# Optimization experiments

Hardware: AMD Instinct MI355X
Metric: run time of the kernel (lower is better)

Reference implementation:

```python
import jax, jax.numpy as jnp
import numpy as np

TOKENS = 64
IN_F = 8192
OUT_F = 8192
CODESZ = 8
CB_SIZE = 256


def fwht(x):
    """Sylvester fast Walsh-Hadamard transform along last dim. x: (B, n), n power of 2."""
    b, n = x.shape
    h = 1
    while h < n:
        x = x.reshape(b, n // (2 * h), 2, h)
        x = jnp.concatenate([x[:, :, :1] + x[:, :, 1:], x[:, :, :1] - x[:, :, 1:]], axis=2)
        x = x.reshape(b, n)
        h *= 2
    return x


def setup_inputs() -> dict:
    key = jax.random.key(0)
    k0, k1, k2, k3, k4, k5 = jax.random.split(key, 6)
    x = jax.random.normal(k0, (TOKENS, IN_F), jnp.float32)
    # SU/SV are random sign vectors in QuIP
    SU = jnp.sign(jax.random.normal(k1, (IN_F,), jnp.float32))
    SV = jnp.sign(jax.random.normal(k2, (OUT_F,), jnp.float32))
    grid = jax.random.normal(k3, (CB_SIZE, CODESZ), jnp.float32)  # codebook entries
    Wscale = jnp.ones((1,), jnp.float32)
    bias = jax.random.normal(k4, (OUT_F,), jnp.float32) * 0.01
    Qidxs = jax.random.randint(k5, (OUT_F, IN_F // CODESZ), 0, CB_SIZE, jnp.int32)
    return {"x": x, "SU": SU, "SV": SV, "grid": grid, "Wscale": Wscale, "bias": bias, "Qidxs": Qidxs}


def reference(x, SU, SV, grid, Wscale, bias, Qidxs):
    # 1) input sign scale
    xs = x * SU
    # 2) matmul_hadUt with folded wscale: x @ H^T / sqrt(n_in) * wscale (H symmetric Sylvester)
    inv_sqrt_in = 1.0 / jnp.sqrt(jnp.asarray(IN_F, x.dtype))
    xh = fwht(xs) * (inv_sqrt_in * Wscale[0])
    # 3) codebook dequant + matmul: W_hat[o, i] from codebook lookup, out = xh @ W_hat^T
    W_hat = grid[Qidxs].reshape(OUT_F, IN_F)  # (out, in) dequantized weight
    y = xh @ W_hat.T  # (tokens, out)
    # 4) matmul_hadU on the output side, truncate to out_features (no-op here: q_out == out)
    inv_sqrt_out = 1.0 / jnp.sqrt(jnp.asarray(OUT_F, x.dtype))
    yh = fwht(y) * inv_sqrt_out
    yh = yh[..., :OUT_F]
    # 5) output sign scale + bias
    return yh * SV + bias
```

## Files before the change

### kernel.cpp

```cpp
#include <hip/hip_runtime.h>
#include <hip/hip_bf16.h>

#define TOKENS 64
#define IN_F 8192
#define OUT_F 8192
#define CB 256

typedef _Float16 half8 __attribute__((ext_vector_type(8)));
typedef float f32x4 __attribute__((ext_vector_type(4)));

__global__ __launch_bounds__(256) void k_fwht_in(const float* __restrict__ x,
                                                 const float* __restrict__ SU,
                                                 const float* __restrict__ Wscale,
                                                 _Float16* __restrict__ xh_frag)
{
    __shared__ float buf[256 * 33];
    __shared__ _Float16 xrowP[256 * 40];
    const int t    = threadIdx.x;
    const int lane = t & 63;
    const int w    = t >> 6;
    const int row  = blockIdx.x;

    float v[32];
    const float* xr = x + row * IN_F;
#pragma unroll
    for (int r = 0; r < 32; ++r) {
        int e = r * 256 + t;
        v[r] = xr[e] * SU[e];
    }
#pragma unroll
    for (int h = 1; h < 32; h <<= 1) {
#pragma unroll
        for (int r = 0; r < 32; ++r) {
            if ((r & h) == 0) {
                float a = v[r], b = v[r + h];
                v[r] = a + b;
                v[r + h] = a - b;
            }
        }
    }
#pragma unroll
    for (int m = 1; m < 64; m <<= 1) {
        bool upper = (lane & m) != 0;
#pragma unroll
        for (int r = 0; r < 32; ++r) {
            float p = __shfl_xor(v[r], m, 64);
            v[r] = upper ? (p - v[r]) : (v[r] + p);
        }
    }
#pragma unroll
    for (int r = 0; r < 32; ++r) buf[t * 33 + r] = v[r];
    __syncthreads();
    {
        float s1 = (w & 1) ? -1.f : 1.f;
        float s2 = (w & 2) ? -1.f : 1.f;
        float s3 = s1 * s2;
#pragma unroll
        for (int r = 0; r < 32; ++r) {
            float a0 = buf[(0 * 64 + lane) * 33 + r];
            float a1 = buf[(1 * 64 + lane) * 33 + r];
            float a2 = buf[(2 * 64 + lane) * 33 + r];
            float a3 = buf[(3 * 64 + lane) * 33 + r];
            v[r] = a0 + s1 * a1 + s2 * a2 + s3 * a3;
        }
    }
    const float scale = 0.011048543456039806f * Wscale[0];
#pragma unroll
    for (int r = 0; r < 32; ++r) {
        int idx = (t & 31) + (r * 8 + (t >> 5)) * 40;
        xrowP[idx] = (_Float16)(v[r] * scale);
    }
    __syncthreads();
    {
        const int mt  = row >> 4;
        const int l15 = row & 15;
        _Float16* base = xh_frag + ((size_t)(t * 4 + mt) * 64 + l15) * 8;
#pragma unroll
        for (int g = 0; g < 4; ++g) {
            half8 val = *(const half8*)&xrowP[t * 40 + g * 8];
            *(half8*)(base + g * 16 * 8) = val;
        }
    }
}

#define SQ_STRIDE 261
__global__ __launch_bounds__(256, 2) void k_qgemm(const _Float16* __restrict__ xh_frag,
                                                  const int* __restrict__ Qidxs,
                                                  const float* __restrict__ grid,
                                                  float* __restrict__ y_part)
{
    __shared__ __align__(16) _Float16 glds[CB * 8];
    __shared__ __align__(16) char uni[4 * 64 * 68 * 4];
    int*   sq  = (int*)uni;
    float* red = (float*)uni;

    const int tid = threadIdx.x;
    const int g   = blockIdx.x >> 2;
    const int p   = blockIdx.x & 3;
    const int n0  = g * 64;

    {
        const float4* gp = (const float4*)grid + tid * 2;
        float4 g0 = gp[0];
        float4 g1 = gp[1];
        _Float16* gl = &glds[tid * 8];
        gl[0] = (_Float16)g0.x; gl[1] = (_Float16)g0.y;
        gl[2] = (_Float16)g0.z; gl[3] = (_Float16)g0.w;
        gl[4] = (_Float16)g1.x; gl[5] = (_Float16)g1.y;
        gl[6] = (_Float16)g1.z; gl[7] = (_Float16)g1.w;
    }
#pragma unroll
    for (int i = 0; i < 16; ++i) {
        int idx4 = i * 256 + tid;
        int r  = idx4 >> 6;
        int c4 = idx4 & 63;
        int4 vv = *(const int4*)(Qidxs + (size_t)(n0 + r) * 1024 + p * 256 + c4 * 4);
        int* dst = &sq[r * SQ_STRIDE + c4 * 4];
        dst[0] = vv.x; dst[1] = vv.y; dst[2] = vv.z; dst[3] = vv.w;
    }
    __syncthreads();

    const int lane = tid & 63;
    const int w    = tid >> 6;
    const int col  = lane & 15;
    const int quad = lane >> 4;

    const int cbase = w * 64 + quad;
#define QGATHER(dst4, s)                                              \
    {                                                                 \
        int cc = cbase + (s) * 4;                                     \
        dst4.x = sq[(0 * 16 + col) * SQ_STRIDE + cc];                 \
        dst4.y = sq[(1 * 16 + col) * SQ_STRIDE + cc];                 \
        dst4.z = sq[(2 * 16 + col) * SQ_STRIDE + cc];                 \
        dst4.w = sq[(3 * 16 + col) * SQ_STRIDE + cc];                 \
    }

    const _Float16* abase = xh_frag + ((size_t)(p * 64 + w * 16) * 4 * 64 + lane) * 8;

    f32x4 acc[4][4] = {};

    int4 qv1, qv2;
    half8 b_c[4];
    {
        int4 qv0;
        QGATHER(qv0, 0);
        QGATHER(qv1, 1);
        QGATHER(qv2, 2);
        b_c[0] = *(const half8*)&glds[qv0.x * 8];
        b_c[1] = *(const half8*)&glds[qv0.y * 8];
        b_c[2] = *(const half8*)&glds[qv0.z * 8];
        b_c[3] = *(const half8*)&glds[qv0.w * 8];
    }
    half8 a_c[4], a_n[4];
#pragma unroll
    for (int mt = 0; mt < 4; ++mt) {
        a_c[mt] = *(const half8*)(abase + (size_t)(0 * 4 + mt) * 512);
        a_n[mt] = *(const half8*)(abase + (size_t)(1 * 4 + mt) * 512);
    }

#pragma unroll 4
    for (int s = 0; s < 16; ++s) {
        const int s3 = (s + 3 < 16 ? s + 3 : 15);
        const int s2 = (s + 2 < 16 ? s + 2 : 15);
        int4 qn;
        QGATHER(qn, s3);
        half8 b_n[4], a_nn[4];
        b_n[0] = *(const half8*)&glds[qv1.x * 8];
        b_n[1] = *(const half8*)&glds[qv1.y * 8];
        b_n[2] = *(const half8*)&glds[qv1.z * 8];
        b_n[3] = *(const half8*)&glds[qv1.w * 8];
#pragma unroll
        for (int mt = 0; mt < 4; ++mt)
            a_nn[mt] = *(const half8*)(abase + (size_t)(s2 * 4 + mt) * 512);
#pragma unroll
        for (int nt = 0; nt < 4; ++nt)
#pragma unroll
            for (int mt = 0; mt < 4; ++mt)
                acc[nt][mt] = __builtin_amdgcn_mfma_f32_16x16x32_f16(
                    a_c[mt], b_c[nt], acc[nt][mt], 0, 0, 0);
#pragma unroll
        for (int nt = 0; nt < 4; ++nt) b_c[nt] = b_n[nt];
        qv1 = qv2; qv2 = qn;
#pragma unroll
        for (int mt = 0; mt < 4; ++mt) { a_c[mt] = a_n[mt]; a_n[mt] = a_nn[mt]; }
    }

    __syncthreads();
#pragma unroll
    for (int nt = 0; nt < 4; ++nt)
#pragma unroll
        for (int mt = 0; mt < 4; ++mt)
#pragma unroll
            for (int i = 0; i < 4; ++i) {
                int r = mt * 16 + quad * 4 + i;
                int c = nt * 16 + col;
                red[(w * 64 + r) * 68 + c] = acc[nt][mt][i];
            }
    __syncthreads();
    float* yp = y_part + (size_t)p * TOKENS * OUT_F;
#pragma unroll
    for (int j = 0; j < 16; ++j) {
        int idx = j * 256 + tid;
        int rr = idx >> 6, cc = idx & 63;
        float s = (red[(0 * 64 + rr) * 68 + cc] + red[(1 * 64 + rr) * 68 + cc])
                + (red[(2 * 64 + rr) * 68 + cc] + red[(3 * 64 + rr) * 68 + cc]);
        yp[(size_t)rr * OUT_F + n0 + cc] = s;
    }
#undef QGATHER
}

__global__ __launch_bounds__(256) void k_fwht_out(const float* __restrict__ y_part,
                                                  const float* __restrict__ SV,
                                                  const float* __restrict__ bias,
                                                  float* __restrict__ out)
{
    __shared__ float buf[256 * 33];
    const int t    = threadIdx.x;
    const int lane = t & 63;
    const int w    = t >> 6;
    const int row  = blockIdx.x;

    const float* y0 = y_part + (size_t)row * OUT_F;
    const size_t ps = (size_t)TOKENS * OUT_F;

    float v[32];
#pragma unroll
    for (int r = 0; r < 32; ++r) {
        int e = r * 256 + t;
        v[r] = (y0[e] + y0[e + ps]) + (y0[e + 2 * ps] + y0[e + 3 * ps]);
    }
#pragma unroll
    for (int h = 1; h < 32; h <<= 1) {
#pragma unroll
        for (int r = 0; r < 32; ++r) {
            if ((r & h) == 0) {
                float a = v[r], b = v[r + h];
                v[r] = a + b;
                v[r + h] = a - b;
            }
        }
    }
#pragma unroll
    for (int m = 1; m < 64; m <<= 1) {
        bool upper = (lane & m) != 0;
#pragma unroll
        for (int r = 0; r < 32; ++r) {
            float p = __shfl_xor(v[r], m, 64);
            v[r] = upper ? (p - v[r]) : (v[r] + p);
        }
    }
#pragma unroll
    for (int r = 0; r < 32; ++r) buf[t * 33 + r] = v[r];
    __syncthreads();
    {
        float s1 = (w & 1) ? -1.f : 1.f;
        float s2 = (w & 2) ? -1.f : 1.f;
        float s3 = s1 * s2;
#pragma unroll
        for (int r = 0; r < 32; ++r) {
            float a0 = buf[(0 * 64 + lane) * 33 + r];
            float a1 = buf[(1 * 64 + lane) * 33 + r];
            float a2 = buf[(2 * 64 + lane) * 33 + r];
            float a3 = buf[(3 * 64 + lane) * 33 + r];
            v[r] = a0 + s1 * a1 + s2 * a2 + s3 * a3;
        }
    }
    const float scale = 0.011048543456039806f;
    float* oo = out + (size_t)row * OUT_F;
#pragma unroll
    for (int r = 0; r < 32; ++r) {
        int e = r * 256 + t;
        oo[e] = v[r] * scale * SV[e] + bias[e];
    }
}

extern "C" void kernel_launch(void* const* d_in, const int* in_sizes, int n_in,
                              void* d_out, int out_size, void* d_ws, size_t ws_size,
                              hipStream_t stream) {
    const float* x      = (const float*)d_in[0];
    const float* SU     = (const float*)d_in[1];
    const float* SV     = (const float*)d_in[2];
    const float* grid   = (const float*)d_in[3];
    const float* Wscale = (const float*)d_in[4];
    const float* bias   = (const float*)d_in[5];
    const int*   Qidxs  = (const int*)d_in[6];
    float* out = (float*)d_out;

    _Float16* xh_frag = (_Float16*)d_ws;
    float*    y_part  = (float*)((char*)d_ws + ((size_t)1 << 20));

    k_fwht_in<<<TOKENS, 256, 0, stream>>>(x, SU, Wscale, xh_frag);
    k_qgemm<<<512, 256, 0, stream>>>(xh_frag, Qidxs, grid, y_part);
    k_fwht_out<<<TOKENS, 256, 0, stream>>>(y_part, SV, bias, out);
}
```

Baseline: 114.2 us.

## Stream Qidxs into per-wave LDS ring during MFMA loop, vectorize FWHT I/O

The quantized GEMM no longer loads the whole Qidxs tile into shared memory behind a block barrier before computing. Each wave now fetches its own rows through a small register ring and writes each slice into a private shared-memory region just before it is gathered, so global index loads overlap with MFMA work. The input and output FWHT kernels switch to float4 loads and stores, using a bit-permuted element-to-register mapping that the Hadamard structure tolerates. The risks are more register pressure from the ring and reliance on intra-wave ordering of shared-memory writes and reads without a barrier.

```diff
diff --git a/kernel.cpp b/kernel.cpp
--- a/kernel.cpp
+++ b/kernel.cpp
@@ -24,9 +24,14 @@
     float v[32];
     const float* xr = x + row * IN_F;
 #pragma unroll
-    for (int r = 0; r < 32; ++r) {
-        int e = r * 256 + t;
-        v[r] = xr[e] * SU[e];
+    for (int rh = 0; rh < 8; ++rh) {
+        int base = (rh << 10) | (t << 2);
+        float4 xv = *(const float4*)(xr + base);
+        float4 sv = *(const float4*)(SU + base);
+        v[rh * 4 + 0] = xv.x * sv.x;
+        v[rh * 4 + 1] = xv.y * sv.y;
+        v[rh * 4 + 2] = xv.z * sv.z;
+        v[rh * 4 + 3] = xv.w * sv.w;
     }
 #pragma unroll
     for (int h = 1; h < 32; h <<= 1) {
@@ -67,7 +72,8 @@
     const float scale = 0.011048543456039806f * Wscale[0];
 #pragma unroll
     for (int r = 0; r < 32; ++r) {
-        int idx = (t & 31) + (r * 8 + (t >> 5)) * 40;
+        int c = ((r >> 2) << 10) | (t << 2) | (r & 3);
+        int idx = (c & 31) + (c >> 5) * 40;
         xrowP[idx] = (_Float16)(v[r] * scale);
     }
     __syncthreads();
@@ -83,14 +89,14 @@
     }
 }
 
-#define SQ_STRIDE 261
+#define SQW 68
 __global__ __launch_bounds__(256, 2) void k_qgemm(const _Float16* __restrict__ xh_frag,
                                                   const int* __restrict__ Qidxs,
                                                   const float* __restrict__ grid,
                                                   float* __restrict__ y_part)
 {
     __shared__ __align__(16) _Float16 glds[CB * 8];
-    __shared__ __align__(16) char uni[4 * 64 * 68 * 4];
+    __shared__ __align__(16) char uni[4 * 64 * SQW * 4];
     int*   sq  = (int*)uni;
     float* red = (float*)uni;
 
@@ -98,6 +104,20 @@
     const int g   = blockIdx.x >> 2;
     const int p   = blockIdx.x & 3;
     const int n0  = g * 64;
+
+    const int lane = tid & 63;
+    const int w    = tid >> 6;
+    const int col  = lane & 15;
+    const int quad = lane >> 4;
+
+    int* sqw = sq + w * (64 * SQW);
+    const int* qsrc = Qidxs + (size_t)(n0 + lane) * 1024 + p * 256 + w * 64;
+
+    int4 ring[4];
+    ring[0] = *(const int4*)(qsrc + 0);
+    ring[1] = *(const int4*)(qsrc + 4);
+    ring[2] = *(const int4*)(qsrc + 8);
+    ring[3] = *(const int4*)(qsrc + 12);
 
     {
         const float4* gp = (const float4*)grid + tid * 2;
@@ -109,30 +129,23 @@
         gl[4] = (_Float16)g1.x; gl[5] = (_Float16)g1.y;
         gl[6] = (_Float16)g1.z; gl[7] = (_Float16)g1.w;
     }
-#pragma unroll
-    for (int i = 0; i < 16; ++i) {
-        int idx4 = i * 256 + tid;
-        int r  = idx4 >> 6;
-        int c4 = idx4 & 63;
-        int4 vv = *(const int4*)(Qidxs + (size_t)(n0 + r) * 1024 + p * 256 + c4 * 4);
-        int* dst = &sq[r * SQ_STRIDE + c4 * 4];
-        dst[0] = vv.x; dst[1] = vv.y; dst[2] = vv.z; dst[3] = vv.w;
-    }
-    __syncthreads();
-
-    const int lane = tid & 63;
-    const int w    = tid >> 6;
-    const int col  = lane & 15;
-    const int quad = lane >> 4;
-
-    const int cbase = w * 64 + quad;
-#define QGATHER(dst4, s)                                              \
+    __syncthreads();
+
+    {
+        int4* dst = (int4*)&sqw[lane * SQW];
+        dst[0] = ring[0];
+        dst[1] = ring[1];
+        dst[2] = ring[2];
+    }
+    ring[0] = *(const int4*)(qsrc + 16);
+
+#define QGATHER(dst4, s_)                                             \
     {                                                                 \
-        int cc = cbase + (s) * 4;                                     \
-        dst4.x = sq[(0 * 16 + col) * SQ_STRIDE + cc];                 \
-        dst4.y = sq[(1 * 16 + col) * SQ_STRIDE + cc];                 \
-        dst4.z = sq[(2 * 16 + col) * SQ_STRIDE + cc];                 \
-        dst4.w = sq[(3 * 16 + col) * SQ_STRIDE + cc];                 \
+        int cc = (s_) * 4 + quad;                                     \
+        dst4.x = sqw[(0 * 16 + col) * SQW + cc];                      \
+        dst4.y = sqw[(1 * 16 + col) * SQW + cc];                      \
+        dst4.z = sqw[(2 * 16 + col) * SQW + cc];                      \
+        dst4.w = sqw[(3 * 16 + col) * SQW + cc];                      \
     }
 
     const _Float16* abase = xh_frag + ((size_t)(p * 64 + w * 16) * 4 * 64 + lane) * 8;
@@ -158,10 +171,42 @@
         a_n[mt] = *(const half8*)(abase + (size_t)(1 * 4 + mt) * 512);
     }
 
-#pragma unroll 4
-    for (int s = 0; s < 16; ++s) {
-        const int s3 = (s + 3 < 16 ? s + 3 : 15);
-        const int s2 = (s + 2 < 16 ? s + 2 : 15);
+#pragma unroll
+    for (int s = 0; s < 12; ++s) {
+        const int s3 = s + 3;
+        const int s2 = s + 2;
+        const int s5 = (s + 5 < 16) ? s + 5 : 15;
+        *(int4*)&sqw[lane * SQW + s3 * 4] = ring[s3 & 3];
+        ring[(s + 1) & 3] = *(const int4*)(qsrc + s5 * 4);
+        int4 qn;
+        QGATHER(qn, s3);
+        half8 b_n[4], a_nn[4];
+        b_n[0] = *(const half8*)&glds[qv1.x * 8];
+        b_n[1] = *(const half8*)&glds[qv1.y * 8];
+        b_n[2] = *(const half8*)&glds[qv1.z * 8];
+        b_n[3] = *(const half8*)&glds[qv1.w * 8];
+#pragma unroll
+        for (int mt = 0; mt < 4; ++mt)
+            a_nn[mt] = *(const half8*)(abase + (size_t)(s2 * 4 + mt) * 512);
+#pragma unroll
+        for (int nt = 0; nt < 4; ++nt)
+#pragma unroll
+            for (int mt = 0; mt < 4; ++mt)
+                acc[nt][mt] = __builtin_amdgcn_mfma_f32_16x16x32_f16(
+                    a_c[mt], b_c[nt], acc[nt][mt], 0, 0, 0);
+#pragma unroll
+        for (int nt = 0; nt < 4; ++nt) b_c[nt] = b_n[nt];
+        qv1 = qv2; qv2 = qn;
+#pragma unroll
+        for (int mt = 0; mt < 4; ++mt) { a_c[mt] = a_n[mt]; a_n[mt] = a_nn[mt]; }
+    }
+
+#pragma unroll
+    for (int s = 12; s < 16; ++s) {
+        const int s3 = 15;
+        const int s2 = (s + 2 < 16) ? s + 2 : 15;
+        if (s == 12)
+            *(int4*)&sqw[lane * SQW + 15 * 4] = ring[3];
         int4 qn;
         QGATHER(qn, s3);
         half8 b_n[4], a_nn[4];
@@ -225,9 +270,16 @@
 
     float v[32];
 #pragma unroll
-    for (int r = 0; r < 32; ++r) {
-        int e = r * 256 + t;
-        v[r] = (y0[e] + y0[e + ps]) + (y0[e + 2 * ps] + y0[e + 3 * ps]);
+    for (int rh = 0; rh < 8; ++rh) {
+        int base = (rh << 10) | (t << 2);
+        float4 a = *(const float4*)(y0 + base);
+        float4 b = *(const float4*)(y0 + ps + base);
+        float4 c = *(const float4*)(y0 + 2 * ps + base);
+        float4 d = *(const float4*)(y0 + 3 * ps + base);
+        v[rh * 4 + 0] = (a.x + b.x) + (c.x + d.x);
+        v[rh * 4 + 1] = (a.y + b.y) + (c.y + d.y);
+        v[rh * 4 + 2] = (a.z + b.z) + (c.z + d.z);
+        v[rh * 4 + 3] = (a.w + b.w) + (c.w + d.w);
     }
 #pragma unroll
     for (int h = 1; h < 32; h <<= 1) {
@@ -268,9 +320,16 @@
     const float scale = 0.011048543456039806f;
     float* oo = out + (size_t)row * OUT_F;
 #pragma unroll
-    for (int r = 0; r < 32; ++r) {
-        int e = r * 256 + t;
-        oo[e] = v[r] * scale * SV[e] + bias[e];
+    for (int rh = 0; rh < 8; ++rh) {
+        int base = (rh << 10) | (t << 2);
+        float4 sv = *(const float4*)(SV + base);
+        float4 bv = *(const float4*)(bias + base);
+        float4 o;
+        o.x = v[rh * 4 + 0] * scale * sv.x + bv.x;
+        o.y = v[rh * 4 + 1] * scale * sv.y + bv.y;
+        o.z = v[rh * 4 + 2] * scale * sv.z + bv.z;
+        o.w = v[rh * 4 + 3] * scale * sv.w + bv.w;
+        *(float4*)(oo + base) = o;
     }
 }
 
```

Result: slower. 136.1 us (+19.2%).
